# Kernel tuning notes

Measured on AMD Instinct MI355X. Metric: run time of the kernel, lower is better.

Reference implementation:

```python
import jax, jax.numpy as jnp
import numpy as np

B, L, N = 8, 5, 4096
RADIUS, K = 0.7, 32
SPATIAL_STRIDE = 16
TK, TSTRIDE = 3, 2  # temporal kernel / stride; temporal_padding=[1,1] replicate
DIM, DEPTH, HEADS, DIM_HEAD, MLP_DIM, OUT_DIM = 512, 5, 8, 64, 1024, 1088
INNER = HEADS * DIM_HEAD
N_ANCH = 64
NTOT = N + N_ANCH
M = NTOT // SPATIAL_STRIDE  # spatial anchors per output frame


def setup_inputs() -> dict:
    key = jax.random.key(0)
    ks = list(jax.random.split(key, 16))
    s = 0.02
    p = {}
    p["points"] = jax.random.uniform(ks[0], (B, L, N, 3), jnp.float32, -1.0, 1.0)
    p["conv_d_w"] = jax.random.normal(ks[1], (DIM, 4), jnp.float32) * s
    p["conv_f_w"] = jax.random.normal(ks[2], (DIM, 3), jnp.float32) * s
    p["pos_w"] = jax.random.normal(ks[3], (DIM, 4), jnp.float32) * s
    p["pos_b"] = jnp.zeros((DIM,), jnp.float32)
    p["ln1_g"] = jnp.ones((DEPTH, DIM)); p["ln1_b"] = jnp.zeros((DEPTH, DIM))
    p["qkv_w"] = jax.random.normal(ks[4], (DEPTH, DIM, 3 * INNER), jnp.float32) * s
    p["attn_out_w"] = jax.random.normal(ks[5], (DEPTH, INNER, DIM), jnp.float32) * s
    p["attn_out_b"] = jnp.zeros((DEPTH, DIM))
    p["ln2_g"] = jnp.ones((DEPTH, DIM)); p["ln2_b"] = jnp.zeros((DEPTH, DIM))
    p["ff1_w"] = jax.random.normal(ks[6], (DEPTH, DIM, MLP_DIM), jnp.float32) * s
    p["ff1_b"] = jnp.zeros((DEPTH, MLP_DIM))
    p["ff2_w"] = jax.random.normal(ks[7], (DEPTH, MLP_DIM, DIM), jnp.float32) * s
    p["ff2_b"] = jnp.zeros((DEPTH, DIM))
    p["head_ln_g"] = jnp.ones((DIM,)); p["head_ln_b"] = jnp.zeros((DIM,))
    p["head1_w"] = jax.random.normal(ks[8], (DIM, MLP_DIM), jnp.float32) * s
    p["head1_b"] = jnp.zeros((MLP_DIM,))
    p["head2_w"] = jax.random.normal(ks[9], (MLP_DIM, OUT_DIM), jnp.float32) * s
    p["head2_b"] = jnp.zeros((OUT_DIM,))
    return p


def _layer_norm(x, g, b, eps=1e-5):
    mu = jnp.mean(x, -1, keepdims=True)
    var = jnp.mean((x - mu) ** 2, -1, keepdims=True)
    return (x - mu) * jax.lax.rsqrt(var + eps) * g + b


def _anchor_grid():
    lin = jnp.linspace(-1.5, 1.5, 4)
    gx, gy, gz = jnp.meshgrid(lin, lin, lin, indexing="ij")
    return jnp.stack([gx.ravel(), gy.ravel(), gz.ravel()], -1)  # (64,3)


def _fps(pts, m):
    # furthest point sampling, pts (N,3) -> (m,) int32, first pick is index 0 (pointnet2 semantics)
    def step(carry, _):
        dist, last = carry
        d = jnp.sum((pts - pts[last]) ** 2, -1)
        dist = jnp.minimum(dist, d)
        return (dist, jnp.argmax(dist).astype(jnp.int32)), last
    init = (jnp.full((pts.shape[0],), 1e10, pts.dtype), jnp.int32(0))
    _, idx = jax.lax.scan(step, init, None, length=m)
    return idx


def _ball_query(anchors, pts, radius, k):
    # first k point indices within radius of each anchor; pad with first hit (0 if none)
    d2 = jnp.sum((anchors[:, None, :] - pts[None, :, :]) ** 2, -1)  # (M,N)
    n = pts.shape[0]
    cand = jnp.where(d2 < radius * radius, jnp.arange(n, dtype=jnp.int32), n)
    neg_topk, _ = jax.lax.top_k(-cand, k)  # k smallest indices, ascending
    idx = -neg_topk
    first = idx[:, :1]
    idx = jnp.where(idx == n, first, idx)
    return jnp.where(idx == n, 0, idx)


def _forward(points, conv_d_w, conv_f_w, pos_w, pos_b, ln1_g, ln1_b, qkv_w,
             attn_out_w, attn_out_b, ln2_g, ln2_b, ff1_w, ff1_b, ff2_w, ff2_b,
             head_ln_g, head_ln_b, head1_w, head1_b, head2_w, head2_b):
    anch = _anchor_grid()  # (64,3)
    pts = jnp.concatenate(
        [points[..., :3], jnp.broadcast_to(anch, (B, L, N_ANCH, 3))], axis=2)  # (B,L,NTOT,3)
    # replicate temporal padding [1,1]
    frames = jnp.concatenate([pts[:, :1], pts, pts[:, -1:]], axis=1)  # (B,L+2,NTOT,3)

    trad = (TK - 1) // 2
    nT = L + 2
    gather = jax.vmap(lambda p, i: p[i])
    out_xyz, out_feat = [], []
    for t in range(trad, nT - trad, TSTRIDE):
        f_t = frames[:, t]                                   # (B,NTOT,3)
        a_idx = jax.vmap(lambda p: _fps(p, M))(f_t)          # (B,M)
        a_xyz = gather(f_t, a_idx)                           # (B,M,3)
        feats_w = []
        for i in range(t - trad, t + trad + 1):
            nb = frames[:, i]                                # (B,NTOT,3)
            idx = jax.vmap(lambda a, p: _ball_query(a, p, RADIUS, K))(a_xyz, nb)  # (B,M,K)
            grouped = gather(nb, idx)                        # (B,M,K,3)
            disp = grouped - a_xyz[:, :, None, :]
            tdisp = jnp.full((B, M, K, 1), float(i - t), disp.dtype)
            disp4 = jnp.concatenate([disp, tdisp], -1)       # (B,M,K,4)
            # conv_f(features) + conv_d(displacement); features fed in are the xyz themselves
            feat = (jnp.einsum("bmkc,dc->bmkd", grouped, conv_f_w)
                    + jnp.einsum("bmkc,dc->bmkd", disp4, conv_d_w))
            feats_w.append(jnp.max(feat, axis=2))            # spatial max -> (B,M,DIM)
        out_feat.append(jnp.max(jnp.stack(feats_w, 0), axis=0))  # temporal max
        out_xyz.append(a_xyz)

    nF = len(out_xyz)
    xyzs = jnp.stack(out_xyz, 1)                             # (B,nF,M,3)
    feats = jnp.stack(out_feat, 1).reshape(B, nF * M, DIM)
    tcol = jnp.broadcast_to(
        jnp.arange(1, nF + 1, dtype=xyzs.dtype)[None, :, None, None], (B, nF, M, 1))
    xyzts = jnp.concatenate([xyzs, tcol], -1).reshape(B, nF * M, 4)
    x = jnp.einsum("bnc,dc->bnd", xyzts, pos_w) + pos_b + feats  # (B,T,DIM); emb_relu=False

    scale = DIM_HEAD ** -0.5
    for l in range(DEPTH):
        xn = _layer_norm(x, ln1_g[l], ln1_b[l])
        q, k, v = jnp.split(xn @ qkv_w[l], 3, axis=-1)
        rs = lambda a: a.reshape(B, -1, HEADS, DIM_HEAD)
        q, k, v = rs(q), rs(k), rs(v)
        att = jax.nn.softmax(jnp.einsum("bqhd,bkhd->bhqk", q, k) * scale, axis=-1)
        o = jnp.einsum("bhqk,bkhd->bqhd", att, v).reshape(B, -1, INNER)
        x = x + o @ attn_out_w[l] + attn_out_b[l]
        xn = _layer_norm(x, ln2_g[l], ln2_b[l])
        x = x + jax.nn.gelu(xn @ ff1_w[l] + ff1_b[l], approximate=False) @ ff2_w[l] + ff2_b[l]

    x = jnp.max(x, axis=1)                                   # (B,DIM)
    x = _layer_norm(x, head_ln_g, head_ln_b)
    x = jax.nn.gelu(x @ head1_w + head1_b, approximate=False) @ head2_w + head2_b
    x = x.reshape(B, 1, OUT_DIM // 64, 64)
    x = jax.nn.softmax(x, axis=-1)
    return x @ anch                                          # (B,1,J,3)


def reference(points, conv_d_w, conv_f_w, pos_w, pos_b, ln1_g, ln1_b, qkv_w,
              attn_out_w, attn_out_b, ln2_g, ln2_b, ff1_w, ff1_b, ff2_w, ff2_b,
              head_ln_g, head_ln_b, head1_w, head1_b, head2_w, head2_b):
    return _forward(points, conv_d_w, conv_f_w, pos_w, pos_b, ln1_g, ln1_b, qkv_w,
                    attn_out_w, attn_out_b, ln2_g, ln2_b, ff1_w, ff1_b, ff2_w, ff2_b,
                    head_ln_g, head_ln_b, head1_w, head1_b, head2_w, head2_b)
```

## Files before the change

kernel.cpp:

```cpp
#include <hip/hip_runtime.h>
#include <hip/hip_bf16.h>
#include <cstddef>

#define BB 8
#define LL 5
#define NN 4096
#define NANCH 64
#define NPTS 4160
#define MM 260
#define NFRAME 3
#define SSEQ 780
#define DIMC 512
#define NHEAD 8
#define DHEAD 64
#define MLPD 1024
#define OUTD 1088
#define NROWS 6240
#define VPITCH 784

typedef __attribute__((ext_vector_type(8))) short s16x8;
typedef __attribute__((ext_vector_type(4))) float fx4;
typedef unsigned short ushort_t;
typedef unsigned int uint_t;

__device__ __forceinline__ float sqdist_rn(float x1, float y1, float z1,
                                           float x2, float y2, float z2) {
    float dx = __fsub_rn(x1, x2);
    float dy = __fsub_rn(y1, y2);
    float dz = __fsub_rn(z1, z2);
    return __fadd_rn(__fadd_rn(__fmul_rn(dx, dx), __fmul_rn(dy, dy)), __fmul_rn(dz, dz));
}

__device__ __forceinline__ float gelu_exact(float v) {
    return 0.5f * v * (1.0f + erff(v * 0.70710678118654752440f));
}

__device__ __forceinline__ uint_t bf16rn(float f) {
    uint_t u = __float_as_uint(f);
    return (u + 0x7FFFu + ((u >> 16) & 1u)) >> 16;
}
__device__ __forceinline__ void split2(float f, ushort_t& h, ushort_t& l) {
    uint_t hb = bf16rn(f);
    h = (ushort_t)hb;
    float fh = __uint_as_float(hb << 16);
    l = (ushort_t)bf16rn(f - fh);
}

template <int CTRL>
__device__ __forceinline__ int dpp_mov(int v) {
    return __builtin_amdgcn_update_dpp(0, v, CTRL, 0xF, 0xF, true);
}
#define DPP_STEP_F(op, v, ctrl) v = op(v, __int_as_float(dpp_mov<ctrl>(__float_as_int(v))))
__device__ __forceinline__ float wave_max_bcast(float v) {
    DPP_STEP_F(fmaxf, v, 0x111); DPP_STEP_F(fmaxf, v, 0x112);
    DPP_STEP_F(fmaxf, v, 0x114); DPP_STEP_F(fmaxf, v, 0x118);
    DPP_STEP_F(fmaxf, v, 0x142); DPP_STEP_F(fmaxf, v, 0x143);
    return __int_as_float(__builtin_amdgcn_readlane(__float_as_int(v), 63));
}
__device__ __forceinline__ float faddf(float a, float b) { return a + b; }
__device__ __forceinline__ float wave_sum_bcast(float v) {
    DPP_STEP_F(faddf, v, 0x111); DPP_STEP_F(faddf, v, 0x112);
    DPP_STEP_F(faddf, v, 0x114); DPP_STEP_F(faddf, v, 0x118);
    DPP_STEP_F(faddf, v, 0x142); DPP_STEP_F(faddf, v, 0x143);
    return __int_as_float(__builtin_amdgcn_readlane(__float_as_int(v), 63));
}
#define DPP_STEP_I(v, ctrl) { int _x = dpp_mov<ctrl>(v); v = v > _x ? v : _x; }
__device__ __forceinline__ int wave_maxi_bcast(int v) {
    DPP_STEP_I(v, 0x111); DPP_STEP_I(v, 0x112);
    DPP_STEP_I(v, 0x114); DPP_STEP_I(v, 0x118);
    DPP_STEP_I(v, 0x142); DPP_STEP_I(v, 0x143);
    return __builtin_amdgcn_readlane(v, 63);
}

__global__ __launch_bounds__(256) void build_pts_kernel(const float* __restrict__ points,
                                                        float* __restrict__ pts) {
    int i = blockIdx.x * 256 + threadIdx.x;
    if (i >= BB * LL * NPTS) return;
    int n = i % NPTS;
    int bl = i / NPTS;
    if (n < NN) {
        const float* src = points + ((size_t)bl * NN + n) * 3;
        pts[(size_t)i * 3 + 0] = src[0];
        pts[(size_t)i * 3 + 1] = src[1];
        pts[(size_t)i * 3 + 2] = src[2];
    } else {
        int j = n - NN;
        int ix = j >> 4, iy = (j >> 2) & 3, iz = j & 3;
        pts[(size_t)i * 3 + 0] = -1.5f + (float)ix;
        pts[(size_t)i * 3 + 1] = -1.5f + (float)iy;
        pts[(size_t)i * 3 + 2] = -1.5f + (float)iz;
    }
}

__global__ __launch_bounds__(256) void fps_kernel(const float* __restrict__ pts,
                                                  float* __restrict__ axyz) {
    int blk = blockIdx.x;
    int b = blk / 3, f = blk % 3;
    const float* P = pts + (size_t)(b * LL + 2 * f) * NPTS * 3;
    int tid = threadIdx.x;
    int lane = tid & 63, wid = tid >> 6;
    const int PPT = 17;
    __shared__ float sx[NPTS], sy[NPTS], sz[NPTS];
    __shared__ float redv[2][4];
    __shared__ int redi[2][4];
    float px[PPT], py[PPT], pz[PPT], dist[PPT];
#pragma unroll
    for (int j = 0; j < PPT; j++) {
        int n = tid + 256 * j;
        if (n < NPTS) {
            float gx = P[(size_t)n * 3 + 0];
            float gy = P[(size_t)n * 3 + 1];
            float gz = P[(size_t)n * 3 + 2];
            px[j] = gx; py[j] = gy; pz[j] = gz;
            sx[n] = gx; sy[n] = gy; sz[n] = gz;
            dist[j] = 1e10f;
        } else {
            px[j] = 0.f; py[j] = 0.f; pz[j] = 0.f;
            dist[j] = -1.0f;
        }
    }
    __syncthreads();
    float ax = sx[0], ay = sy[0], az = sz[0];
    float* out = axyz + (size_t)blk * MM * 3;
    for (int m = 0; m < MM; m++) {
        if (tid == 0) { out[m * 3 + 0] = ax; out[m * 3 + 1] = ay; out[m * 3 + 2] = az; }
        float bestv = -1.0f;
        int bestn = NPTS;
#pragma unroll
        for (int j = 0; j < PPT; j++) {
            int n = tid + 256 * j;
            if (n < NPTS) {
                float d = sqdist_rn(px[j], py[j], pz[j], ax, ay, az);
                float dj = fminf(dist[j], d);
                dist[j] = dj;
                if (dj > bestv) { bestv = dj; bestn = n; }
            }
        }
        float wm = wave_max_bcast(bestv);
        int wn = 0x7FFFFFFF - wave_maxi_bcast(bestv == wm ? (0x7FFFFFFF - bestn) : 0);
        int par = m & 1;
        if (lane == 0) { redv[par][wid] = wm; redi[par][wid] = wn; }
        __syncthreads();
        float bv = redv[par][0];
        int bn = redi[par][0];
#pragma unroll
        for (int w = 1; w < 4; w++) {
            float v2 = redv[par][w]; int i2 = redi[par][w];
            if (v2 > bv || (v2 == bv && i2 < bn)) { bv = v2; bn = i2; }
        }
        ax = sx[bn]; ay = sy[bn]; az = sz[bn];
    }
}

__global__ __launch_bounds__(64) void group_conv_kernel(
    const float* __restrict__ pts, const float* __restrict__ axyz,
    const float* __restrict__ conv_d_w, const float* __restrict__ conv_f_w,
    const float* __restrict__ pos_w, const float* __restrict__ pos_b,
    float* __restrict__ x) {
    int gid = blockIdx.x;
    int b = gid / SSEQ;
    int rem = gid % SSEQ;
    int f = rem / MM;
    int lane = threadIdx.x;
    const float* A = axyz + (size_t)gid * 3;
    float ax = A[0], ay = A[1], az = A[2];

    float cf0[8], cf1[8], cf2[8], cd0[8], cd1[8], cd2[8], cd3[8], fmx[8];
#pragma unroll
    for (int c = 0; c < 8; c++) {
        int d = lane + 64 * c;
        cf0[c] = conv_f_w[d * 3 + 0];
        cf1[c] = conv_f_w[d * 3 + 1];
        cf2[c] = conv_f_w[d * 3 + 2];
        cd0[c] = conv_d_w[d * 4 + 0];
        cd1[c] = conv_d_w[d * 4 + 1];
        cd2[c] = conv_d_w[d * 4 + 2];
        cd3[c] = conv_d_w[d * 4 + 3];
        fmx[c] = -INFINITY;
    }
    __shared__ int nbr[32];
    __shared__ float gxs[32], gys[32], gzs[32];
    const float R2 = 0.49000000953674316f;

    for (int wi = 0; wi < 3; wi++) {
        int l = 2 * f + wi - 1;
        l = l < 0 ? 0 : (l > 4 ? 4 : l);
        const float* P = pts + (size_t)(b * LL + l) * NPTS * 3;
        int cnt = 0;
        for (int base = 0; base < NPTS && cnt < 32; base += 64) {
            int n = base + lane;
            float d2 = sqdist_rn(P[(size_t)n * 3], P[(size_t)n * 3 + 1], P[(size_t)n * 3 + 2],
                                 ax, ay, az);
            bool hit = d2 < R2;
            unsigned long long mk = __ballot(hit);
            int rank = (int)__popcll(mk & (((unsigned long long)1 << lane) - 1ull));
            if (hit && (cnt + rank) < 32) nbr[cnt + rank] = n;
            cnt += (int)__popcll(mk);
        }
        __syncthreads();
        int eff = cnt < 32 ? cnt : 32;
        if (lane < 32) {
            int idx = (eff == 0) ? 0 : (lane < eff ? nbr[lane] : nbr[0]);
            gxs[lane] = P[(size_t)idx * 3 + 0];
            gys[lane] = P[(size_t)idx * 3 + 1];
            gzs[lane] = P[(size_t)idx * 3 + 2];
        }
        __syncthreads();
        float tf = (float)(wi - 1);
        for (int k = 0; k < 32; k++) {
            float gx = gxs[k], gy = gys[k], gz = gzs[k];
            float dx = gx - ax, dy = gy - ay, dz = gz - az;
#pragma unroll
            for (int c = 0; c < 8; c++) {
                float v = gx * cf0[c] + gy * cf1[c] + gz * cf2[c] +
                          dx * cd0[c] + dy * cd1[c] + dz * cd2[c] + tf * cd3[c];
                fmx[c] = fmaxf(fmx[c], v);
            }
        }
        __syncthreads();
    }
    float tcol = (float)(f + 1);
#pragma unroll
    for (int c = 0; c < 8; c++) {
        int d = lane + 64 * c;
        float pos = ax * pos_w[d * 4 + 0] + ay * pos_w[d * 4 + 1] +
                    az * pos_w[d * 4 + 2] + tcol * pos_w[d * 4 + 3] + pos_b[d];
        x[(size_t)gid * DIMC + d] = fmx[c] + pos;
    }
}

__global__ __launch_bounds__(64) void ln_kernel(const float* __restrict__ x,
                                                const float* __restrict__ g,
                                                const float* __restrict__ b,
                                                ushort_t* __restrict__ yh,
                                                ushort_t* __restrict__ yl) {
    int r = blockIdx.x;
    int lane = threadIdx.x;
    const float* xr = x + (size_t)r * DIMC;
    float4 v0 = *(const float4*)(xr + lane * 8);
    float4 v1 = *(const float4*)(xr + lane * 8 + 4);
    float s = v0.x + v0.y + v0.z + v0.w + v1.x + v1.y + v1.z + v1.w;
    s = wave_sum_bcast(s);
    float mean = s * (1.0f / 512.0f);
    float dv[8];
    dv[0] = v0.x - mean; dv[1] = v0.y - mean; dv[2] = v0.z - mean; dv[3] = v0.w - mean;
    dv[4] = v1.x - mean; dv[5] = v1.y - mean; dv[6] = v1.z - mean; dv[7] = v1.w - mean;
    float sq = 0.f;
#pragma unroll
    for (int c = 0; c < 8; c++) sq += dv[c] * dv[c];
    sq = wave_sum_bcast(sq);
    float var = sq * (1.0f / 512.0f);
    float inv = 1.0f / sqrtf(var + 1e-5f);
    int d = lane * 8;
    ushort_t hs[8], ls[8];
#pragma unroll
    for (int c = 0; c < 8; c++) {
        float v = dv[c] * inv * g[d + c] + b[d + c];
        split2(v, hs[c], ls[c]);
    }
    uint4 hv, lv;
    hv.x = hs[0] | ((uint_t)hs[1] << 16); hv.y = hs[2] | ((uint_t)hs[3] << 16);
    hv.z = hs[4] | ((uint_t)hs[5] << 16); hv.w = hs[6] | ((uint_t)hs[7] << 16);
    lv.x = ls[0] | ((uint_t)ls[1] << 16); lv.y = ls[2] | ((uint_t)ls[3] << 16);
    lv.z = ls[4] | ((uint_t)ls[5] << 16); lv.w = ls[6] | ((uint_t)ls[7] << 16);
    *(uint4*)(yh + (size_t)r * DIMC + d) = hv;
    *(uint4*)(yl + (size_t)r * DIMC + d) = lv;
}

__global__ __launch_bounds__(256) void wsplit_kernel(const float* __restrict__ qkvw,
                                                     const float* __restrict__ projw,
                                                     const float* __restrict__ ff1w,
                                                     const float* __restrict__ ff2w,
                                                     ushort_t* __restrict__ th,
                                                     ushort_t* __restrict__ tl) {
    int bid = blockIdx.x;
    const float* src; int K, N; size_t dst;
    if (bid < 768)       { src = qkvw;  K = 512;  N = 1536; dst = 0;       }
    else if (bid < 1024) { src = projw; K = 512;  N = 512;  dst = 786432;  bid -= 768;  }
    else if (bid < 1536) { src = ff1w;  K = 512;  N = 1024; dst = 1048576; bid -= 1024; }
    else                 { src = ff2w;  K = 1024; N = 512;  dst = 1572864; bid -= 1536; }
    int ntn = N >> 5;
    int tn = bid % ntn, tk = bid / ntn;
    int n0 = tn * 32, k0 = tk * 32;
    __shared__ float T[32][33];
    int tid = threadIdx.x;
    int tx = tid & 31, ty = tid >> 5;
#pragma unroll
    for (int i = 0; i < 4; i++)
        T[ty + 8 * i][tx] = src[(size_t)(k0 + ty + 8 * i) * N + n0 + tx];
    __syncthreads();
#pragma unroll
    for (int i = 0; i < 4; i++) {
        int n = n0 + ty + 8 * i;
        int k = k0 + tx;
        ushort_t h, l;
        split2(T[tx][ty + 8 * i], h, l);
        th[dst + (size_t)n * K + k] = h;
        tl[dst + (size_t)n * K + k] = l;
    }
}

#define KP 40

template <int BN, int EPI>
__global__ __launch_bounds__(256, 2) void gemm_mfma(
    const ushort_t* __restrict__ Ahg, const ushort_t* __restrict__ Alg,
    const ushort_t* __restrict__ Bhg, const ushort_t* __restrict__ Blg,
    const float* __restrict__ bias, const float* __restrict__ R,
    float* __restrict__ C, ushort_t* __restrict__ Ch, ushort_t* __restrict__ Cl,
    ushort_t* __restrict__ Vh, ushort_t* __restrict__ Vl,
    int M, int N, int K) {
    const int WN = BN / 2, NT = WN / 16;
    __shared__ ushort_t Ah[128 * KP];
    __shared__ ushort_t Al[128 * KP];
    __shared__ ushort_t Bh[BN * KP];
    __shared__ ushort_t Bl[BN * KP];
    int tid = threadIdx.x;
    int lane = tid & 63, w = tid >> 6;
    int wm = w & 1, wn = w >> 1;
    int quad = lane >> 4, l15 = lane & 15;
    int m0 = blockIdx.y * 128, n0 = blockIdx.x * BN;

    fx4 acc[4][NT];
#pragma unroll
    for (int mi = 0; mi < 4; mi++)
#pragma unroll
        for (int nj = 0; nj < NT; nj++) acc[mi][nj] = (fx4){0.f, 0.f, 0.f, 0.f};

    for (int k0 = 0; k0 < K; k0 += 32) {
#pragma unroll
        for (int i = 0; i < 2; i++) {
            int task = tid + 256 * i;
            int row = task >> 2, kc = (task & 3) * 8;
            if (m0 + row < M) {
                size_t go = (size_t)(m0 + row) * K + k0 + kc;
                *(float4*)&Ah[row * KP + kc] = *(const float4*)(Ahg + go);
                *(float4*)&Al[row * KP + kc] = *(const float4*)(Alg + go);
            }
        }
#pragma unroll
        for (int i = 0; i < BN / 64; i++) {
            int task = tid + 256 * i;
            int row = task >> 2, kc = (task & 3) * 8;
            size_t go = (size_t)(n0 + row) * K + k0 + kc;
            *(float4*)&Bh[row * KP + kc] = *(const float4*)(Bhg + go);
            *(float4*)&Bl[row * KP + kc] = *(const float4*)(Blg + go);
        }
        __syncthreads();
        s16x8 af[4][2], bf[NT][2];
#pragma unroll
        for (int mi = 0; mi < 4; mi++) {
            int off = (64 * wm + 16 * mi + l15) * KP + quad * 8;
            af[mi][0] = *(const s16x8*)&Ah[off];
            af[mi][1] = *(const s16x8*)&Al[off];
        }
#pragma unroll
        for (int nj = 0; nj < NT; nj++) {
            int off = (WN * wn + 16 * nj + l15) * KP + quad * 8;
            bf[nj][0] = *(const s16x8*)&Bh[off];
            bf[nj][1] = *(const s16x8*)&Bl[off];
        }
#pragma unroll
        for (int mi = 0; mi < 4; mi++)
#pragma unroll
            for (int nj = 0; nj < NT; nj++) {
                acc[mi][nj] = __builtin_amdgcn_mfma_f32_16x16x32_bf16(af[mi][0], bf[nj][0], acc[mi][nj], 0, 0, 0);
                acc[mi][nj] = __builtin_amdgcn_mfma_f32_16x16x32_bf16(af[mi][0], bf[nj][1], acc[mi][nj], 0, 0, 0);
                acc[mi][nj] = __builtin_amdgcn_mfma_f32_16x16x32_bf16(af[mi][1], bf[nj][0], acc[mi][nj], 0, 0, 0);
            }
        __syncthreads();
    }
#pragma unroll
    for (int mi = 0; mi < 4; mi++) {
#pragma unroll
        for (int r = 0; r < 4; r++) {
            int row = m0 + 64 * wm + 16 * mi + quad * 4 + r;
            if (row < M) {
#pragma unroll
                for (int nj = 0; nj < NT; nj++) {
                    int col = n0 + WN * wn + 16 * nj + l15;
                    float v = acc[mi][nj][r];
                    if (EPI == 0) {
                        C[(size_t)row * N + col] = v;
                    } else if (EPI == 3) {
                        C[(size_t)row * N + col] = v + bias[col] + R[(size_t)row * N + col];
                    } else if (EPI == 2) {
                        float gv = gelu_exact(v + bias[col]);
                        ushort_t h, l;
                        split2(gv, h, l);
                        Ch[(size_t)row * N + col] = h;
                        Cl[(size_t)row * N + col] = l;
                    } else if (EPI == 5) {
                        ushort_t h, l;
                        split2(v, h, l);
                        if (col < 1024) {
                            Ch[(size_t)row * 1024 + col] = h;
                            Cl[(size_t)row * 1024 + col] = l;
                        } else {
                            int bb = row / SSEQ, key = row % SSEQ;
                            int hh = (col - 1024) >> 6, dd = (col - 1024) & 63;
                            size_t vo = ((size_t)((bb * 8 + hh) * 64 + dd)) * VPITCH + key;
                            Vh[vo] = h;
                            Vl[vo] = l;
                        }
                    }
                }
            }
        }
    }
}

#define AP 72

__global__ __launch_bounds__(256, 2) void attn_mfma_kernel(
    const ushort_t* __restrict__ qkh, const ushort_t* __restrict__ qkl,
    const ushort_t* __restrict__ vth, const ushort_t* __restrict__ vtl,
    ushort_t* __restrict__ oh, ushort_t* __restrict__ ol) {
    int qt = blockIdx.x, h = blockIdx.y, b = blockIdx.z;
    int tid = threadIdx.x;
    int lane = tid & 63, w = tid >> 6;
    int quad = lane >> 4, l15 = lane & 15;
    int bh = b * 8 + h;

    __shared__ __align__(16) ushort_t Qh[64 * AP], Ql[64 * AP];
    __shared__ __align__(16) ushort_t Kh[64 * AP], Kl[64 * AP];
    __shared__ __align__(16) ushort_t Vth[64 * AP], Vtl[64 * AP];
    __shared__ __align__(16) ushort_t Ph[64 * AP], Pl[64 * AP];

    int q0 = qt * 64;
    int nq = SSEQ - q0; if (nq > 64) nq = 64;

#pragma unroll
    for (int i = 0; i < 2; i++) {
        int t = tid + 256 * i;
        int row = t >> 3, c = (t & 7) * 8;
        int gq = q0 + (row < nq ? row : nq - 1);
        size_t go = (size_t)(b * SSEQ + gq) * 1024 + h * 64 + c;
        *(uint4*)&Qh[row * AP + c] = *(const uint4*)(qkh + go);
        *(uint4*)&Ql[row * AP + c] = *(const uint4*)(qkl + go);
    }

    fx4 accO[4];
#pragma unroll
    for (int dj = 0; dj < 4; dj++) accO[dj] = (fx4){0.f, 0.f, 0.f, 0.f};
    fx4 accL = (fx4){0.f, 0.f, 0.f, 0.f};

    s16x8 ones;
#pragma unroll
    for (int j = 0; j < 8; j++) ones[j] = (short)16256;

    for (int kt = 0; kt < 13; kt++) {
        int k0 = kt * 64;
        int nk = SSEQ - k0; if (nk > 64) nk = 64;
        __syncthreads();
#pragma unroll
        for (int i = 0; i < 2; i++) {
            int t = tid + 256 * i;
            int row = t >> 3, c = (t & 7) * 8;
            int gk = k0 + (row < nk ? row : nk - 1);
            size_t go = (size_t)(b * SSEQ + gk) * 1024 + h * 64 + c;
            *(uint4*)&Kh[row * AP + c] = *(const uint4*)(qkh + go + 512);
            *(uint4*)&Kl[row * AP + c] = *(const uint4*)(qkl + go + 512);
            size_t vo = ((size_t)(bh * 64 + row)) * VPITCH + k0 + c;
            *(uint4*)&Vth[row * AP + c] = *(const uint4*)(vth + vo);
            *(uint4*)&Vtl[row * AP + c] = *(const uint4*)(vtl + vo);
        }
        __syncthreads();

        fx4 accS[4];
#pragma unroll
        for (int nj = 0; nj < 4; nj++) accS[nj] = (fx4){0.f, 0.f, 0.f, 0.f};
#pragma unroll
        for (int ks = 0; ks < 2; ks++) {
            s16x8 aH = *(const s16x8*)&Qh[(16 * w + l15) * AP + 32 * ks + quad * 8];
            s16x8 aL = *(const s16x8*)&Ql[(16 * w + l15) * AP + 32 * ks + quad * 8];
#pragma unroll
            for (int nj = 0; nj < 4; nj++) {
                s16x8 bH = *(const s16x8*)&Kh[(16 * nj + l15) * AP + 32 * ks + quad * 8];
                s16x8 bL = *(const s16x8*)&Kl[(16 * nj + l15) * AP + 32 * ks + quad * 8];
                accS[nj] = __builtin_amdgcn_mfma_f32_16x16x32_bf16(aH, bH, accS[nj], 0, 0, 0);
                accS[nj] = __builtin_amdgcn_mfma_f32_16x16x32_bf16(aH, bL, accS[nj], 0, 0, 0);
                accS[nj] = __builtin_amdgcn_mfma_f32_16x16x32_bf16(aL, bH, accS[nj], 0, 0, 0);
            }
        }
#pragma unroll
        for (int nj = 0; nj < 4; nj++) {
            int key = 16 * nj + l15;
            bool valid = key < nk;
#pragma unroll
            for (int r = 0; r < 4; r++) {
                float s = accS[nj][r] * 0.125f;
                float p = valid ? __expf(s) : 0.f;
                ushort_t hh, ll;
                split2(p, hh, ll);
                int qrow = 16 * w + quad * 4 + r;
                Ph[qrow * AP + key] = hh;
                Pl[qrow * AP + key] = ll;
            }
        }
#pragma unroll
        for (int ks = 0; ks < 2; ks++) {
            s16x8 aPh = *(const s16x8*)&Ph[(16 * w + l15) * AP + 32 * ks + quad * 8];
            s16x8 aPl = *(const s16x8*)&Pl[(16 * w + l15) * AP + 32 * ks + quad * 8];
            accL = __builtin_amdgcn_mfma_f32_16x16x32_bf16(aPh, ones, accL, 0, 0, 0);
            accL = __builtin_amdgcn_mfma_f32_16x16x32_bf16(aPl, ones, accL, 0, 0, 0);
#pragma unroll
            for (int dj = 0; dj < 4; dj++) {
                s16x8 bVh = *(const s16x8*)&Vth[(16 * dj + l15) * AP + 32 * ks + quad * 8];
                s16x8 bVl = *(const s16x8*)&Vtl[(16 * dj + l15) * AP + 32 * ks + quad * 8];
                accO[dj] = __builtin_amdgcn_mfma_f32_16x16x32_bf16(aPh, bVh, accO[dj], 0, 0, 0);
                accO[dj] = __builtin_amdgcn_mfma_f32_16x16x32_bf16(aPh, bVl, accO[dj], 0, 0, 0);
                accO[dj] = __builtin_amdgcn_mfma_f32_16x16x32_bf16(aPl, bVh, accO[dj], 0, 0, 0);
            }
        }
    }
#pragma unroll
    for (int r = 0; r < 4; r++) {
        int lq = 16 * w + quad * 4 + r;
        if (lq < nq) {
            float inv = 1.0f / accL[r];
            size_t base = (size_t)(b * SSEQ + q0 + lq) * DIMC + h * 64 + l15;
#pragma unroll
            for (int dj = 0; dj < 4; dj++) {
                ushort_t hh, ll;
                split2(accO[dj][r] * inv, hh, ll);
                oh[base + 16 * dj] = hh;
                ol[base + 16 * dj] = ll;
            }
        }
    }
}

__global__ __launch_bounds__(512) void pool_max_kernel(const float* __restrict__ x,
                                                       float* __restrict__ partial) {
    int c = blockIdx.x;
    int bb = blockIdx.y;
    int d = threadIdx.x;
    const float* xb = x + ((size_t)(bb * SSEQ + c * 60)) * DIMC + d;
    float m = -INFINITY;
#pragma unroll 4
    for (int s = 0; s < 60; s++) m = fmaxf(m, xb[(size_t)s * DIMC]);
    partial[((size_t)bb * 13 + c) * DIMC + d] = m;
}

__global__ __launch_bounds__(512) void pool_ln_kernel(const float* __restrict__ partial,
                                                      const float* __restrict__ g,
                                                      const float* __restrict__ b,
                                                      float* __restrict__ out) {
    int bb = blockIdx.x;
    int d = threadIdx.x;
    const float* pb = partial + (size_t)bb * 13 * DIMC + d;
    float m = -INFINITY;
#pragma unroll
    for (int c = 0; c < 13; c++) m = fmaxf(m, pb[(size_t)c * DIMC]);
    __shared__ float col[512];
    __shared__ float red[512];
    col[d] = m;
    red[d] = m;
    __syncthreads();
    for (int s = 256; s > 0; s >>= 1) {
        if (d < s) red[d] += red[d + s];
        __syncthreads();
    }
    float mean = red[0] * (1.0f / 512.0f);
    __syncthreads();
    float dv = col[d] - mean;
    red[d] = dv * dv;
    __syncthreads();
    for (int s = 256; s > 0; s >>= 1) {
        if (d < s) red[d] += red[d + s];
        __syncthreads();
    }
    float var = red[0] * (1.0f / 512.0f);
    float inv = 1.0f / sqrtf(var + 1e-5f);
    out[(size_t)bb * DIMC + d] = dv * inv * g[d] + b[d];
}

__global__ __launch_bounds__(256) void head1_kernel(const float* __restrict__ in,
                                                    const float* __restrict__ W,
                                                    const float* __restrict__ bias,
                                                    float* __restrict__ out) {
    int g = blockIdx.x, bb = blockIdx.y;
    int tid = threadIdx.x;
    int c = tid & 63, ks = tid >> 6;
    int col = g * 64 + c;
    __shared__ float xr[512];
    xr[tid] = in[(size_t)bb * 512 + tid];
    xr[tid + 256] = in[(size_t)bb * 512 + tid + 256];
    __syncthreads();
    float acc = 0.f;
    const float* Wc = W + col;
    for (int k = ks * 128; k < ks * 128 + 128; k++)
        acc += xr[k] * Wc[(size_t)k * MLPD];
    __shared__ float red[256];
    red[tid] = acc;
    __syncthreads();
    if (ks == 0) {
        float v = red[c] + red[c + 64] + red[c + 128] + red[c + 192] + bias[col];
        out[(size_t)bb * MLPD + col] = gelu_exact(v);
    }
}

__global__ __launch_bounds__(256) void head2_kernel(const float* __restrict__ in,
                                                    const float* __restrict__ W,
                                                    const float* __restrict__ bias,
                                                    float* __restrict__ out) {
    int g = blockIdx.x, bb = blockIdx.y;
    int tid = threadIdx.x;
    int c = tid & 63, ks = tid >> 6;
    int col = g * 64 + c;
    __shared__ float xr[1024];
    xr[tid] = in[(size_t)bb * 1024 + tid];
    xr[tid + 256] = in[(size_t)bb * 1024 + tid + 256];
    xr[tid + 512] = in[(size_t)bb * 1024 + tid + 512];
    xr[tid + 768] = in[(size_t)bb * 1024 + tid + 768];
    __syncthreads();
    float acc = 0.f;
    const float* Wc = W + col;
    for (int k = ks * 256; k < ks * 256 + 256; k++)
        acc += xr[k] * Wc[(size_t)k * OUTD];
    __shared__ float red[256];
    red[tid] = acc;
    __syncthreads();
    if (ks == 0) {
        out[(size_t)bb * OUTD + col] = red[c] + red[c + 64] + red[c + 128] + red[c + 192] + bias[col];
    }
}

__global__ __launch_bounds__(64) void smax_anchor_kernel(const float* __restrict__ h2,
                                                         float* __restrict__ out) {
    int bb = blockIdx.x / 17;
    int gcol = blockIdx.x % 17;
    int j = threadIdx.x;
    float v = h2[(size_t)bb * OUTD + gcol * 64 + j];
    float mx = wave_max_bcast(v);
    float p = expf(v - mx);
    float sum = wave_sum_bcast(p);
    int ix = j >> 4, iy = (j >> 2) & 3, iz = j & 3;
    float sx = wave_sum_bcast(p * (-1.5f + (float)ix));
    float sy = wave_sum_bcast(p * (-1.5f + (float)iy));
    float sz = wave_sum_bcast(p * (-1.5f + (float)iz));
    if (j == 0) {
        float* o = out + ((size_t)bb * 17 + gcol) * 3;
        o[0] = sx / sum;
        o[1] = sy / sum;
        o[2] = sz / sum;
    }
}

extern "C" void kernel_launch(void* const* d_in, const int* in_sizes, int n_in,
                              void* d_out, int out_size, void* d_ws, size_t ws_size,
                              hipStream_t stream) {
    const float* points     = (const float*)d_in[0];
    const float* conv_d_w   = (const float*)d_in[1];
    const float* conv_f_w   = (const float*)d_in[2];
    const float* pos_w      = (const float*)d_in[3];
    const float* pos_b      = (const float*)d_in[4];
    const float* ln1_g      = (const float*)d_in[5];
    const float* ln1_b      = (const float*)d_in[6];
    const float* qkv_w      = (const float*)d_in[7];
    const float* attn_out_w = (const float*)d_in[8];
    const float* attn_out_b = (const float*)d_in[9];
    const float* ln2_g      = (const float*)d_in[10];
    const float* ln2_b      = (const float*)d_in[11];
    const float* ff1_w      = (const float*)d_in[12];
    const float* ff1_b      = (const float*)d_in[13];
    const float* ff2_w      = (const float*)d_in[14];
    const float* ff2_b      = (const float*)d_in[15];
    const float* head_ln_g  = (const float*)d_in[16];
    const float* head_ln_b  = (const float*)d_in[17];
    const float* head1_w    = (const float*)d_in[18];
    const float* head1_b    = (const float*)d_in[19];
    const float* head2_w    = (const float*)d_in[20];
    const float* head2_b    = (const float*)d_in[21];

    float* ws = (float*)d_ws;
    float* pts    = ws;
    float* axyz   = pts + 499200;
    float* xbuf   = axyz + 18720;
    float* qkvreg = xbuf + 3194880;
    float* pooled = qkvreg + 9601024;
    float* h1     = pooled + 4096;
    float* h2     = h1 + 8192;
    float* fend   = h2 + 8704;
    ushort_t* qkh = (ushort_t*)qkvreg;
    ushort_t* qkl = qkh + 6389760;
    ushort_t* vth = qkl + 6389760;
    ushort_t* vtl = vth + 3211264;
    ushort_t* us   = (ushort_t*)fend;
    ushort_t* xnh  = us;
    ushort_t* xnl  = xnh + 3194880;
    ushort_t* atth = xnl + 3194880;
    ushort_t* attl = atth + 3194880;
    ushort_t* ffhh = attl + 3194880;
    ushort_t* ffhl = ffhh + 6389760;
    ushort_t* wth  = ffhl + 6389760;
    ushort_t* wtl  = wth + 2097152;
    float* ppart = qkvreg;

    build_pts_kernel<<<650, 256, 0, stream>>>(points, pts);
    fps_kernel<<<24, 256, 0, stream>>>(pts, axyz);
    group_conv_kernel<<<NROWS, 64, 0, stream>>>(pts, axyz, conv_d_w, conv_f_w,
                                                pos_w, pos_b, xbuf);
    const int MB = (NROWS + 127) / 128;
    for (int l = 0; l < 5; l++) {
        wsplit_kernel<<<2048, 256, 0, stream>>>(
            qkv_w + (size_t)l * 512 * 1536, attn_out_w + (size_t)l * 512 * 512,
            ff1_w + (size_t)l * 512 * 1024, ff2_w + (size_t)l * 1024 * 512, wth, wtl);
        ln_kernel<<<NROWS, 64, 0, stream>>>(xbuf, ln1_g + l * 512, ln1_b + l * 512, xnh, xnl);
        gemm_mfma<128, 5><<<dim3(1536 / 128, MB), 256, 0, stream>>>(
            xnh, xnl, wth, wtl, nullptr, nullptr, nullptr, qkh, qkl, vth, vtl,
            NROWS, 1536, 512);
        attn_mfma_kernel<<<dim3(13, NHEAD, BB), 256, 0, stream>>>(qkh, qkl, vth, vtl,
                                                                  atth, attl);
        gemm_mfma<64, 3><<<dim3(512 / 64, MB), 256, 0, stream>>>(
            atth, attl, wth + 786432, wtl + 786432, attn_out_b + l * 512, xbuf,
            xbuf, nullptr, nullptr, nullptr, nullptr, NROWS, 512, 512);
        ln_kernel<<<NROWS, 64, 0, stream>>>(xbuf, ln2_g + l * 512, ln2_b + l * 512, xnh, xnl);
        gemm_mfma<128, 2><<<dim3(1024 / 128, MB), 256, 0, stream>>>(
            xnh, xnl, wth + 1048576, wtl + 1048576, ff1_b + l * 1024, nullptr,
            nullptr, ffhh, ffhl, nullptr, nullptr, NROWS, 1024, 512);
        gemm_mfma<64, 3><<<dim3(512 / 64, MB), 256, 0, stream>>>(
            ffhh, ffhl, wth + 1572864, wtl + 1572864, ff2_b + l * 512, xbuf,
            xbuf, nullptr, nullptr, nullptr, nullptr, NROWS, 512, 1024);
    }
    pool_max_kernel<<<dim3(13, BB), 512, 0, stream>>>(xbuf, ppart);
    pool_ln_kernel<<<BB, 512, 0, stream>>>(ppart, head_ln_g, head_ln_b, pooled);
    head1_kernel<<<dim3(16, BB), 256, 0, stream>>>(pooled, head1_w, head1_b, h1);
    head2_kernel<<<dim3(17, BB), 256, 0, stream>>>(h1, head2_w, head2_b, h2);
    smax_anchor_kernel<<<BB * 17, 64, 0, stream>>>(h2, (float*)d_out);
}
```

Measured before the change: 2.027 ms.

## Overlap weight splitting with FPS and attention kernels via double-buffered weights

Drops the separate per-layer weight split kernel. Layer 0 weights are now split by extra blocks in the FPS launch, and each next layer's weights are split by extra blocks in the current layer's attention launch, using two ping-pong weight buffers. FPS also moves from 256 to 1024 threads per block with a 16-way reduction tree, cutting the serial per-point work on its 24 blocks. The goal is to hide weight conversion behind under-occupied kernels and to save launches. The cost is more memory for the second weight buffer, and the larger static shared memory in the fused kernels may lower occupancy.

```diff
diff --git a/kernel.cpp b/kernel.cpp
--- a/kernel.cpp
+++ b/kernel.cpp
@@ -17,6 +17,7 @@
 #define OUTD 1088
 #define NROWS 6240
 #define VPITCH 784
+#define WBUFSZ 2097152
 
 typedef __attribute__((ext_vector_type(8))) short s16x8;
 typedef __attribute__((ext_vector_type(4))) float fx4;
@@ -70,6 +71,34 @@
     DPP_STEP_I(v, 0x114); DPP_STEP_I(v, 0x118);
     DPP_STEP_I(v, 0x142); DPP_STEP_I(v, 0x143);
     return __builtin_amdgcn_readlane(v, 63);
+}
+
+__device__ __forceinline__ void wsplit_tile(
+    int bid, int tid, int nthr,
+    const float* __restrict__ qkvw, const float* __restrict__ projw,
+    const float* __restrict__ ff1w, const float* __restrict__ ff2w,
+    ushort_t* __restrict__ th, ushort_t* __restrict__ tl,
+    float (*T)[33]) {
+    const float* src; int K, N; size_t dst;
+    if (bid < 768)       { src = qkvw;  K = 512;  N = 1536; dst = 0;       }
+    else if (bid < 1024) { src = projw; K = 512;  N = 512;  dst = 786432;  bid -= 768;  }
+    else if (bid < 1536) { src = ff1w;  K = 512;  N = 1024; dst = 1048576; bid -= 1024; }
+    else                 { src = ff2w;  K = 1024; N = 512;  dst = 1572864; bid -= 1536; }
+    int ntn = N >> 5;
+    int tn = bid % ntn, tk = bid / ntn;
+    int n0 = tn * 32, k0 = tk * 32;
+    for (int e = tid; e < 1024; e += nthr) {
+        int r = e >> 5, c = e & 31;
+        T[r][c] = src[(size_t)(k0 + r) * N + n0 + c];
+    }
+    __syncthreads();
+    for (int e = tid; e < 1024; e += nthr) {
+        int r = e >> 5, c = e & 31;
+        ushort_t h, l;
+        split2(T[c][r], h, l);
+        th[dst + (size_t)(n0 + r) * K + k0 + c] = h;
+        tl[dst + (size_t)(n0 + r) * K + k0 + c] = l;
+    }
 }
 
 __global__ __launch_bounds__(256) void build_pts_kernel(const float* __restrict__ points,
@@ -92,21 +121,33 @@
     }
 }
 
-__global__ __launch_bounds__(256) void fps_kernel(const float* __restrict__ pts,
-                                                  float* __restrict__ axyz) {
-    int blk = blockIdx.x;
-    int b = blk / 3, f = blk % 3;
+__global__ __launch_bounds__(1024) void fps_ws_kernel(
+    const float* __restrict__ pts, float* __restrict__ axyz,
+    const float* __restrict__ qkvw, const float* __restrict__ projw,
+    const float* __restrict__ ff1w, const float* __restrict__ ff2w,
+    ushort_t* __restrict__ th, ushort_t* __restrict__ tl) {
+    __shared__ __align__(16) char smem[50432];
+    int bid = blockIdx.x;
+    int tid = threadIdx.x;
+    if (bid >= 24) {
+        wsplit_tile(bid - 24, tid, 1024, qkvw, projw, ff1w, ff2w, th, tl,
+                    (float(*)[33])smem);
+        return;
+    }
+    float* sx = (float*)smem;
+    float* sy = sx + NPTS;
+    float* sz = sy + NPTS;
+    float* redv = sz + NPTS;
+    int* redi = (int*)(redv + 32);
+
+    int b = bid / 3, f = bid % 3;
     const float* P = pts + (size_t)(b * LL + 2 * f) * NPTS * 3;
-    int tid = threadIdx.x;
     int lane = tid & 63, wid = tid >> 6;
-    const int PPT = 17;
-    __shared__ float sx[NPTS], sy[NPTS], sz[NPTS];
-    __shared__ float redv[2][4];
-    __shared__ int redi[2][4];
+    const int PPT = 5;
     float px[PPT], py[PPT], pz[PPT], dist[PPT];
 #pragma unroll
     for (int j = 0; j < PPT; j++) {
-        int n = tid + 256 * j;
+        int n = tid + 1024 * j;
         if (n < NPTS) {
             float gx = P[(size_t)n * 3 + 0];
             float gy = P[(size_t)n * 3 + 1];
@@ -121,14 +162,14 @@
     }
     __syncthreads();
     float ax = sx[0], ay = sy[0], az = sz[0];
-    float* out = axyz + (size_t)blk * MM * 3;
+    float* out = axyz + (size_t)bid * MM * 3;
     for (int m = 0; m < MM; m++) {
         if (tid == 0) { out[m * 3 + 0] = ax; out[m * 3 + 1] = ay; out[m * 3 + 2] = az; }
         float bestv = -1.0f;
         int bestn = NPTS;
 #pragma unroll
         for (int j = 0; j < PPT; j++) {
-            int n = tid + 256 * j;
+            int n = tid + 1024 * j;
             if (n < NPTS) {
                 float d = sqdist_rn(px[j], py[j], pz[j], ax, ay, az);
                 float dj = fminf(dist[j], d);
@@ -138,16 +179,22 @@
         }
         float wm = wave_max_bcast(bestv);
         int wn = 0x7FFFFFFF - wave_maxi_bcast(bestv == wm ? (0x7FFFFFFF - bestn) : 0);
-        int par = m & 1;
-        if (lane == 0) { redv[par][wid] = wm; redi[par][wid] = wn; }
-        __syncthreads();
-        float bv = redv[par][0];
-        int bn = redi[par][0];
-#pragma unroll
-        for (int w = 1; w < 4; w++) {
-            float v2 = redv[par][w]; int i2 = redi[par][w];
-            if (v2 > bv || (v2 == bv && i2 < bn)) { bv = v2; bn = i2; }
-        }
+        int par = (m & 1) * 16;
+        if (lane == 0) { redv[par + wid] = wm; redi[par + wid] = wn; }
+        __syncthreads();
+        float v[16]; int id[16];
+#pragma unroll
+        for (int k = 0; k < 16; k++) { v[k] = redv[par + k]; id[k] = redi[par + k]; }
+#pragma unroll
+        for (int s = 8; s; s >>= 1)
+#pragma unroll
+            for (int k = 0; k < 8; k++)
+                if (k < s) {
+                    if (v[k + s] > v[k] || (v[k + s] == v[k] && id[k + s] < id[k])) {
+                        v[k] = v[k + s]; id[k] = id[k + s];
+                    }
+                }
+        int bn = id[0];
         ax = sx[bn]; ay = sy[bn]; az = sz[bn];
     }
 }
@@ -265,39 +312,6 @@
     lv.z = ls[4] | ((uint_t)ls[5] << 16); lv.w = ls[6] | ((uint_t)ls[7] << 16);
     *(uint4*)(yh + (size_t)r * DIMC + d) = hv;
     *(uint4*)(yl + (size_t)r * DIMC + d) = lv;
-}
-
-__global__ __launch_bounds__(256) void wsplit_kernel(const float* __restrict__ qkvw,
-                                                     const float* __restrict__ projw,
-                                                     const float* __restrict__ ff1w,
-                                                     const float* __restrict__ ff2w,
-                                                     ushort_t* __restrict__ th,
-                                                     ushort_t* __restrict__ tl) {
-    int bid = blockIdx.x;
-    const float* src; int K, N; size_t dst;
-    if (bid < 768)       { src = qkvw;  K = 512;  N = 1536; dst = 0;       }
-    else if (bid < 1024) { src = projw; K = 512;  N = 512;  dst = 786432;  bid -= 768;  }
-    else if (bid < 1536) { src = ff1w;  K = 512;  N = 1024; dst = 1048576; bid -= 1024; }
-    else                 { src = ff2w;  K = 1024; N = 512;  dst = 1572864; bid -= 1536; }
-    int ntn = N >> 5;
-    int tn = bid % ntn, tk = bid / ntn;
-    int n0 = tn * 32, k0 = tk * 32;
-    __shared__ float T[32][33];
-    int tid = threadIdx.x;
-    int tx = tid & 31, ty = tid >> 5;
-#pragma unroll
-    for (int i = 0; i < 4; i++)
-        T[ty + 8 * i][tx] = src[(size_t)(k0 + ty + 8 * i) * N + n0 + tx];
-    __syncthreads();
-#pragma unroll
-    for (int i = 0; i < 4; i++) {
-        int n = n0 + ty + 8 * i;
-        int k = k0 + tx;
-        ushort_t h, l;
-        split2(T[tx][ty + 8 * i], h, l);
-        th[dst + (size_t)n * K + k] = h;
-        tl[dst + (size_t)n * K + k] = l;
-    }
 }
 
 #define KP 40
@@ -415,17 +429,31 @@
 __global__ __launch_bounds__(256, 2) void attn_mfma_kernel(
     const ushort_t* __restrict__ qkh, const ushort_t* __restrict__ qkl,
     const ushort_t* __restrict__ vth, const ushort_t* __restrict__ vtl,
-    ushort_t* __restrict__ oh, ushort_t* __restrict__ ol) {
+    ushort_t* __restrict__ oh, ushort_t* __restrict__ ol,
+    const float* __restrict__ nqkvw, const float* __restrict__ nprojw,
+    const float* __restrict__ nff1w, const float* __restrict__ nff2w,
+    ushort_t* __restrict__ nth, ushort_t* __restrict__ ntl) {
+    __shared__ __align__(16) char smem[73728];
+    if (blockIdx.x >= 13) {
+        int widx = (blockIdx.x - 13) * 64 + blockIdx.y * 8 + blockIdx.z;
+        wsplit_tile(widx, threadIdx.x, 256, nqkvw, nprojw, nff1w, nff2w,
+                    nth, ntl, (float(*)[33])smem);
+        return;
+    }
+    ushort_t* Qh  = (ushort_t*)smem;
+    ushort_t* Ql  = Qh + 64 * AP;
+    ushort_t* Kh  = Ql + 64 * AP;
+    ushort_t* Kl  = Kh + 64 * AP;
+    ushort_t* Vth = Kl + 64 * AP;
+    ushort_t* Vtl = Vth + 64 * AP;
+    ushort_t* Ph  = Vtl + 64 * AP;
+    ushort_t* Pl  = Ph + 64 * AP;
+
     int qt = blockIdx.x, h = blockIdx.y, b = blockIdx.z;
     int tid = threadIdx.x;
     int lane = tid & 63, w = tid >> 6;
     int quad = lane >> 4, l15 = lane & 15;
     int bh = b * 8 + h;
-
-    __shared__ __align__(16) ushort_t Qh[64 * AP], Ql[64 * AP];
-    __shared__ __align__(16) ushort_t Kh[64 * AP], Kl[64 * AP];
-    __shared__ __align__(16) ushort_t Vth[64 * AP], Vtl[64 * AP];
-    __shared__ __align__(16) ushort_t Ph[64 * AP], Pl[64 * AP];
 
     int q0 = qt * 64;
     int nq = SSEQ - q0; if (nq > 64) nq = 64;
@@ -694,34 +722,43 @@
     ushort_t* attl = atth + 3194880;
     ushort_t* ffhh = attl + 3194880;
     ushort_t* ffhl = ffhh + 6389760;
-    ushort_t* wth  = ffhl + 6389760;
-    ushort_t* wtl  = wth + 2097152;
+    ushort_t* wbh  = ffhl + 6389760;
+    ushort_t* wbl  = wbh + 2 * WBUFSZ;
     float* ppart = qkvreg;
 
     build_pts_kernel<<<650, 256, 0, stream>>>(points, pts);
-    fps_kernel<<<24, 256, 0, stream>>>(pts, axyz);
+    fps_ws_kernel<<<24 + 2048, 1024, 0, stream>>>(
+        pts, axyz, qkv_w, attn_out_w, ff1_w, ff2_w, wbh, wbl);
     group_conv_kernel<<<NROWS, 64, 0, stream>>>(pts, axyz, conv_d_w, conv_f_w,
                                                 pos_w, pos_b, xbuf);
     const int MB = (NROWS + 127) / 128;
     for (int l = 0; l < 5; l++) {
-        wsplit_kernel<<<2048, 256, 0, stream>>>(
-            qkv_w + (size_t)l * 512 * 1536, attn_out_w + (size_t)l * 512 * 512,
-            ff1_w + (size_t)l * 512 * 1024, ff2_w + (size_t)l * 1024 * 512, wth, wtl);
-        ln_kernel<<<NROWS, 64, 0, stream>>>(xbuf, ln1_g + l * 512, ln1_b + l * 512, xnh, xnl);
+        ushort_t* wth = wbh + (size_t)(l & 1) * WBUFSZ;
+        ushort_t* wtl = wbl + (size_t)(l & 1) * WBUFSZ;
+        ushort_t* nth = wbh + (size_t)((l + 1) & 1) * WBUFSZ;
+        ushort_t* ntl = wbl + (size_t)((l + 1) & 1) * WBUFSZ;
+        int ln2off = l * 512;
+        ln_kernel<<<NROWS, 64, 0, stream>>>(xbuf, ln1_g + ln2off, ln1_b + ln2off, xnh, xnl);
         gemm_mfma<128, 5><<<dim3(1536 / 128, MB), 256, 0, stream>>>(
             xnh, xnl, wth, wtl, nullptr, nullptr, nullptr, qkh, qkl, vth, vtl,
             NROWS, 1536, 512);
-        attn_mfma_kernel<<<dim3(13, NHEAD, BB), 256, 0, stream>>>(qkh, qkl, vth, vtl,
-                                                                  atth, attl);
+        int lnx = l + 1;
+        attn_mfma_kernel<<<dim3(l < 4 ? 45 : 13, NHEAD, BB), 256, 0, stream>>>(
+            qkh, qkl, vth, vtl, atth, attl,
+            l < 4 ? qkv_w + (size_t)lnx * 512 * 1536 : nullptr,
+            l < 4 ? attn_out_w + (size_t)lnx * 512 * 512 : nullptr,
+            l < 4 ? ff1_w + (size_t)lnx * 512 * 1024 : nullptr,
+            l < 4 ? ff2_w + (size_t)lnx * 1024 * 512 : nullptr,
+            nth, ntl);
         gemm_mfma<64, 3><<<dim3(512 / 64, MB), 256, 0, stream>>>(
-            atth, attl, wth + 786432, wtl + 786432, attn_out_b + l * 512, xbuf,
+            atth, attl, wth + 786432, wtl + 786432, attn_out_b + ln2off, xbuf,
             xbuf, nullptr, nullptr, nullptr, nullptr, NROWS, 512, 512);
-        ln_kernel<<<NROWS, 64, 0, stream>>>(xbuf, ln2_g + l * 512, ln2_b + l * 512, xnh, xnl);
+        ln_kernel<<<NROWS, 64, 0, stream>>>(xbuf, ln2_g + ln2off, ln2_b + ln2off, xnh, xnl);
         gemm_mfma<128, 2><<<dim3(1024 / 128, MB), 256, 0, stream>>>(
             xnh, xnl, wth + 1048576, wtl + 1048576, ff1_b + l * 1024, nullptr,
             nullptr, ffhh, ffhl, nullptr, nullptr, NROWS, 1024, 512);
         gemm_mfma<64, 3><<<dim3(512 / 64, MB), 256, 0, stream>>>(
-            ffhh, ffhl, wth + 1572864, wtl + 1572864, ff2_b + l * 512, xbuf,
+            ffhh, ffhl, wth + 1572864, wtl + 1572864, ff2_b + ln2off, xbuf,
             xbuf, nullptr, nullptr, nullptr, nullptr, NROWS, 512, 1024);
     }
     pool_max_kernel<<<dim3(13, BB), 512, 0, stream>>>(xbuf, ppart);
```

After: 2.202 ms. 8.6% more time.
